# Kernel tuning notes

Hardware: AMD Instinct MI355X
Metric: run time of the kernel (lower is better)

## Reference

```python
import jax, jax.numpy as jnp
import numpy as np

B, N, C, H, PD, CLN = 8, 1024, 512, 8, 256, 64
HD = C // H
HID = 4 * C
LN_EPS = 1e-5
ATT_EPS = 1e-6


def layernorm(x, g, b):
    mu = x.mean(-1, keepdims=True)
    var = ((x - mu) ** 2).mean(-1, keepdims=True)
    return (x - mu) * jax.lax.rsqrt(var + LN_EPS) * g + b


def setup_inputs() -> dict:
    key = jax.random.key(0)
    ks = jax.random.split(key, 16)
    p = lambda k, shp, s=0.02: (jax.random.normal(k, shp, dtype=jnp.float32) * s)
    return {
        "x_token": jax.random.normal(ks[0], (B, N, C), dtype=jnp.float32),
        "x_path": jax.random.normal(ks[1], (B, N, PD), dtype=jnp.float32),
        "wq": p(ks[2], (C, C)),
        "wk": p(ks[3], (C, C)),
        "wv": p(ks[4], (C, C)),
        "w_proj": p(ks[5], (C, C)),
        "b_proj": jnp.zeros((C,), jnp.float32),
        "g1": jnp.ones((C,), jnp.float32),
        "b1": jnp.zeros((C,), jnp.float32),
        "g2": jnp.ones((C,), jnp.float32),
        "b2": jnp.zeros((C,), jnp.float32),
        "w1": p(ks[6], (HID, C)),
        "bb1": jnp.zeros((HID,), jnp.float32),
        "w2": p(ks[7], (C, HID)),
        "bb2": jnp.zeros((C,), jnp.float32),
        "idx_cluster": jax.random.randint(ks[8], (B, N), 0, CLN, dtype=jnp.int64 if jax.config.jax_enable_x64 else jnp.int32),
        "cluster_num": CLN,
    }


def reference(x_token, x_path, wq, wk, wv, w_proj, b_proj, g1, b1, g2, b2,
              w1, bb1, w2, bb2, idx_cluster, cluster_num):
    Bn, Nn, Cn = x_token.shape
    scale = (Cn // H) ** -0.5

    # norm1 + attention
    t = layernorm(x_token, g1, b1)
    q = (t @ wq.T).reshape(Bn, Nn, H, HD).transpose(0, 2, 1, 3)  # bhnd
    k = (t @ wk.T).reshape(Bn, Nn, H, HD).transpose(0, 2, 1, 3)
    v = (t @ wv.T).reshape(Bn, Nn, H, HD).transpose(0, 2, 1, 3)

    # scatter-to-(B,cluster,N,C) then sum over clusters == same-cluster mask on QK^T
    scores = jnp.einsum("bhid,bhjd->bhij", q, k) * scale  # (B,H,N,N)
    same = (idx_cluster[:, None, :, None] == idx_cluster[:, None, None, :])  # (B,1,N,N)
    scores = jnp.where(same, scores, jnp.float32(-1e9))

    # custom eps-stabilized exp-softmax (as in the torch code, no max-subtraction)
    e = jnp.exp(scores.astype(jnp.float32))
    attn = (e + ATT_EPS / Nn) / (e.sum(-1, keepdims=True) + ATT_EPS)

    out = jnp.einsum("bhij,bhjd->bhid", attn, v)
    out = out.transpose(0, 2, 1, 3).reshape(Bn, Nn, Cn)
    out = out @ w_proj.T + b_proj

    x = x_token + out  # drop_path is identity in eval

    # MLP block
    h = layernorm(x, g2, b2)
    m = jax.nn.gelu(h @ w1.T + bb1, approximate=False) @ w2.T + bb2
    return x + m
```

## Files before the change

kernel.cpp:

```cpp
#include <hip/hip_runtime.h>

typedef unsigned short u16;
typedef __attribute__((ext_vector_type(4))) float f32x4;
typedef __attribute__((ext_vector_type(8))) short s16x8;
typedef __attribute__((ext_vector_type(4))) unsigned short u16x4;
typedef __attribute__((ext_vector_type(8))) unsigned short u16x8;

__device__ __forceinline__ u16 f2bf(float f) {
    unsigned int u = __builtin_bit_cast(unsigned int, f);
    u += 0x7fffu + ((u >> 16) & 1u);
    return (u16)(u >> 16);
}
__device__ __forceinline__ float bf2f(u16 h) {
    unsigned int u = ((unsigned int)h) << 16;
    return __builtin_bit_cast(float, u);
}
__device__ __forceinline__ void gload16(const u16* g, u16* l) {
    __builtin_amdgcn_global_load_lds(
        (const __attribute__((address_space(1))) void*)g,
        (__attribute__((address_space(3))) void*)l, 16, 0, 0);
}
__device__ __forceinline__ float fgelu(float x) {
    float y = 0.7978845608f * (x + 0.044715f * x * x * x);
    float e = __builtin_amdgcn_exp2f(y * 2.8853900817f);
    float th = 1.0f - 2.0f / (1.0f + e);
    return 0.5f * x * (1.0f + th);
}

__global__ __launch_bounds__(256) void cvt_all(const float* __restrict__ wq,
                                               const float* __restrict__ wk,
                                               const float* __restrict__ wv,
                                               const float* __restrict__ wp,
                                               const float* __restrict__ w1,
                                               const float* __restrict__ w2,
                                               u16* __restrict__ dqkv,
                                               u16* __restrict__ dp,
                                               u16* __restrict__ dw1,
                                               u16* __restrict__ dw2,
                                               float* __restrict__ vsum) {
    int b = blockIdx.x;
    if (b >= 3072) {
        float4 z = {0.f, 0.f, 0.f, 0.f};
        ((float4*)vsum)[(b - 3072) * 256 + threadIdx.x] = z;
        return;
    }
    const float* src; u16* dst; int off;
    if      (b < 256)  { src = wq; dst = dqkv;          off = b; }
    else if (b < 512)  { src = wk; dst = dqkv + 262144; off = b - 256; }
    else if (b < 768)  { src = wv; dst = dqkv + 524288; off = b - 512; }
    else if (b < 1024) { src = wp; dst = dp;            off = b - 768; }
    else if (b < 2048) { src = w1; dst = dw1;           off = b - 1024; }
    else               { src = w2; dst = dw2;           off = b - 2048; }
    int i = off * 256 + threadIdx.x;
    float4 v = ((const float4*)src)[i];
    u16x4 o;
    o.x = f2bf(v.x); o.y = f2bf(v.y); o.z = f2bf(v.z); o.w = f2bf(v.w);
    ((u16x4*)dst)[i] = o;
}

__global__ __launch_bounds__(128) void ln_kernel(const float* __restrict__ in,
                                                 const float* __restrict__ g,
                                                 const float* __restrict__ bta,
                                                 u16* __restrict__ out) {
    int row = blockIdx.x;
    int t = threadIdx.x;
    float4 v = ((const float4*)(in + (size_t)row * 512))[t];
    float s  = v.x + v.y + v.z + v.w;
    float s2 = v.x * v.x + v.y * v.y + v.z * v.z + v.w * v.w;
#pragma unroll
    for (int m = 1; m < 64; m <<= 1) { s += __shfl_xor(s, m); s2 += __shfl_xor(s2, m); }
    __shared__ float sh[4];
    if ((t & 63) == 0) { sh[(t >> 6) * 2] = s; sh[(t >> 6) * 2 + 1] = s2; }
    __syncthreads();
    s = sh[0] + sh[2]; s2 = sh[1] + sh[3];
    float mu  = s * (1.0f / 512.0f);
    float var = s2 * (1.0f / 512.0f) - mu * mu;
    float rstd = rsqrtf(var + 1e-5f);
    float4 gv = ((const float4*)g)[t];
    float4 bv = ((const float4*)bta)[t];
    u16x4 o;
    o.x = f2bf((v.x - mu) * rstd * gv.x + bv.x);
    o.y = f2bf((v.y - mu) * rstd * gv.y + bv.y);
    o.z = f2bf((v.z - mu) * rstd * gv.z + bv.z);
    o.w = f2bf((v.w - mu) * rstd * gv.w + bv.w);
    ((u16x4*)(out + (size_t)row * 512))[t] = o;
}

__global__ __launch_bounds__(512) void vsum_part(const u16* __restrict__ qkv,
                                                 float* __restrict__ vsum) {
    int b = blockIdx.x >> 3, chunk = blockIdx.x & 7;
    int c = threadIdx.x;
    const u16* base = qkv + (size_t)b * 1024 * 1536 + 1024 + c;
    float s = 0.0f;
    for (int n = chunk * 128; n < chunk * 128 + 128; ++n) s += bf2f(base[(size_t)n * 1536]);
    atomicAdd(&vsum[b * 512 + c], s);
}

__global__ __launch_bounds__(1024) void cluster_sort(const int* __restrict__ idx,
                                                     int* __restrict__ perm,
                                                     int* __restrict__ cstart,
                                                     int* __restrict__ ccnt) {
    const int b = blockIdx.x, t = threadIdx.x;
    const int w = t >> 6, lane = t & 63;
    __shared__ int whist[16][64];
    __shared__ int cnt[64];
    __shared__ int off[64];
    ((int*)whist)[t] = 0;
    __syncthreads();
    const int myc = idx[b * 1024 + t];
    atomicAdd(&whist[w][myc], 1);
    int rank_w = 0;
    for (int c = 0; c < 64; ++c) {
        unsigned long long m = __ballot(myc == c);
        if (myc == c) rank_w = __popcll(m & ((1ull << lane) - 1ull));
    }
    __syncthreads();
    if (t < 64) {
        int s = 0;
        for (int ww = 0; ww < 16; ++ww) s += whist[ww][t];
        cnt[t] = s;
        ccnt[b * 64 + t] = s;
    }
    __syncthreads();
    if (t == 0) {
        int s = 0;
        for (int c = 0; c < 64; ++c) { off[c] = s; s += cnt[c]; }
    }
    __syncthreads();
    int cross = 0;
    for (int ww = 0; ww < w; ++ww) cross += whist[ww][myc];
    perm[b * 1024 + off[myc] + cross + rank_w] = t;
    if (t < 64) cstart[b * 64 + t] = off[t];
}

__global__ __launch_bounds__(64) void cattn_kernel(const u16* __restrict__ qkv,
                                                   const int* __restrict__ perm,
                                                   const int* __restrict__ cstart,
                                                   const int* __restrict__ ccnt,
                                                   const float* __restrict__ vsum,
                                                   u16* __restrict__ O) {
    const int bid = blockIdx.x;
    const int h = bid & 7, c = (bid >> 3) & 63, b = bid >> 9;
    const int m = ccnt[b * 64 + c];
    if (m == 0) return;
    const int start = b * 1024 + cstart[b * 64 + c];
    const int lane = threadIdx.x;
    const int fr = lane & 15, fkb = lane >> 4;
    __shared__ __align__(16) u16 Qs[16 * 72];
    __shared__ __align__(16) u16 Ks[32 * 72];
    __shared__ __align__(16) u16 Vt[64 * 36];
    __shared__ __align__(16) u16 Pl[16 * 40];

    const u16* qkv_b = qkv + (size_t)b * 1024 * 1536;
    const float epsN = 1e-6f / 1024.0f;

    for (int q0 = 0; q0 < m; q0 += 16) {
        __syncthreads();
        {
            int row = lane >> 3, seg = lane & 7;
#pragma unroll
            for (int p = 0; p < 2; ++p) {
                int r = row + p * 8;
                int gr = perm[start + min(q0 + r, m - 1)];
                *(int4*)(&Qs[r * 72 + seg * 8]) =
                    *(const int4*)(qkv_b + (size_t)gr * 1536 + h * 64 + seg * 8);
            }
        }
        __syncthreads();
        const s16x8 qf0 = *(const s16x8*)(&Qs[fr * 72 + fkb * 8]);
        const s16x8 qf1 = *(const s16x8*)(&Qs[fr * 72 + 32 + fkb * 8]);

        f32x4 oacc[4] = {};
        float rs[4] = {0.f, 0.f, 0.f, 0.f};

        for (int k0 = 0; k0 < m; k0 += 32) {
            __syncthreads();
            {
                int row = lane >> 3, seg = lane & 7;
#pragma unroll
                for (int p = 0; p < 4; ++p) {
                    int r = row + p * 8;
                    int gr = perm[start + min(k0 + r, m - 1)];
                    const u16* src = qkv_b + (size_t)gr * 1536 + h * 64 + seg * 8;
                    *(int4*)(&Ks[r * 72 + seg * 8]) = *(const int4*)(src + 512);
                    u16x8 vv = *(const u16x8*)(src + 1024);
#pragma unroll
                    for (int i = 0; i < 8; ++i) Vt[(seg * 8 + i) * 36 + r] = vv[i];
                }
            }
            __syncthreads();
#pragma unroll
            for (int ct = 0; ct < 2; ++ct) {
                f32x4 sacc = {};
                s16x8 kf0 = *(const s16x8*)(&Ks[(ct * 16 + fr) * 72 + fkb * 8]);
                s16x8 kf1 = *(const s16x8*)(&Ks[(ct * 16 + fr) * 72 + 32 + fkb * 8]);
                sacc = __builtin_amdgcn_mfma_f32_16x16x32_bf16(qf0, kf0, sacc, 0, 0, 0);
                sacc = __builtin_amdgcn_mfma_f32_16x16x32_bf16(qf1, kf1, sacc, 0, 0, 0);
                bool valid = (k0 + ct * 16 + fr) < m;
#pragma unroll
                for (int r = 0; r < 4; ++r) {
                    float e = valid ? __expf(sacc[r] * 0.125f) : 0.0f;
                    rs[r] += e;
                    Pl[(fkb * 4 + r) * 40 + ct * 16 + fr] = f2bf(e);
                }
            }
            __syncthreads();
            s16x8 pf = *(const s16x8*)(&Pl[fr * 40 + fkb * 8]);
#pragma unroll
            for (int dt = 0; dt < 4; ++dt) {
                s16x8 vf = *(const s16x8*)(&Vt[(dt * 16 + fr) * 36 + fkb * 8]);
                oacc[dt] = __builtin_amdgcn_mfma_f32_16x16x32_bf16(pf, vf, oacc[dt], 0, 0, 0);
            }
        }
#pragma unroll
        for (int r = 0; r < 4; ++r)
#pragma unroll
            for (int mm = 1; mm < 16; mm <<= 1) rs[r] += __shfl_xor(rs[r], mm);

#pragma unroll
        for (int r = 0; r < 4; ++r) {
            int ql = q0 + fkb * 4 + r;
            if (ql < m) {
                int orow = perm[start + ql];
#pragma unroll
                for (int dt = 0; dt < 4; ++dt) {
                    int dcol = dt * 16 + fr;
                    float vs = vsum[(b * 8 + h) * 64 + dcol];
                    float val = (oacc[dt][r] + epsN * vs) / (rs[r] + 1e-6f);
                    O[((size_t)(b * 1024 + orow)) * 512 + h * 64 + dcol] = f2bf(val);
                }
            }
        }
    }
}

template <int BM, bool OUT_BF16, bool BIAS, bool RESID, bool GELU>
__global__ __launch_bounds__(256) void gemm_sb(const u16* __restrict__ A,
                                               const u16* __restrict__ W,
                                               const float* __restrict__ bias,
                                               const float* __restrict__ resid,
                                               void* __restrict__ outp,
                                               int M, int N, int K) {
    constexpr int MI = BM / 32;
    __shared__ __align__(16) u16 As[BM * 64];
    __shared__ __align__(16) u16 Bs[128 * 64];
    const int bm = blockIdx.x, bn = blockIdx.y;
    const int t = threadIdx.x;
    const int lane = t & 63, w = t >> 6;
    const int wm = w >> 1, wn = w & 1;
    const int fr = lane & 15, fkb = lane >> 4;
    const int l8 = lane >> 3;
    const int c8s = (((lane & 7) ^ (l8 & 7)) * 8);
    f32x4 acc[MI][4] = {};
    const u16* Ab = A + (size_t)bm * BM * K;
    const u16* Wb = W + (size_t)bn * 128 * K;

    for (int k0 = 0; k0 < K; k0 += 64) {
        __syncthreads();
#pragma unroll
        for (int j = 0; j < MI; ++j) {
            int r = (w * MI + j) * 8 + l8;
            gload16(Ab + (size_t)r * K + k0 + c8s, &As[(w * MI + j) * 512]);
        }
#pragma unroll
        for (int j = 0; j < 4; ++j) {
            int r = (w * 4 + j) * 8 + l8;
            gload16(Wb + (size_t)r * K + k0 + c8s, &Bs[(w * 4 + j) * 512]);
        }
        __syncthreads();
#pragma unroll
        for (int kk = 0; kk < 64; kk += 32) {
            const int co = (((kk >> 3) + fkb) ^ (fr & 7)) << 3;
            s16x8 af[MI], bfv[4];
#pragma unroll
            for (int mi = 0; mi < MI; ++mi)
                af[mi] = *(const s16x8*)(&As[(wm * (BM / 2) + mi * 16 + fr) * 64 + co]);
#pragma unroll
            for (int ni = 0; ni < 4; ++ni)
                bfv[ni] = *(const s16x8*)(&Bs[(wn * 64 + ni * 16 + fr) * 64 + co]);
#pragma unroll
            for (int mi = 0; mi < MI; ++mi)
#pragma unroll
                for (int ni = 0; ni < 4; ++ni)
                    acc[mi][ni] = __builtin_amdgcn_mfma_f32_16x16x32_bf16(
                        bfv[ni], af[mi], acc[mi][ni], 0, 0, 0);
        }
    }

    const int rg = (lane >> 4) * 4;
#pragma unroll
    for (int mi = 0; mi < MI; ++mi) {
        const int grow = bm * BM + wm * (BM / 2) + mi * 16 + fr;
#pragma unroll
        for (int ni = 0; ni < 4; ++ni) {
            const int gcol = bn * 128 + wn * 64 + ni * 16 + rg;
            const size_t base = (size_t)grow * N + gcol;
            float4 v;
            v.x = acc[mi][ni][0]; v.y = acc[mi][ni][1];
            v.z = acc[mi][ni][2]; v.w = acc[mi][ni][3];
            if (BIAS) {
                float4 bv = *(const float4*)(bias + gcol);
                v.x += bv.x; v.y += bv.y; v.z += bv.z; v.w += bv.w;
            }
            if (GELU) {
                v.x = fgelu(v.x); v.y = fgelu(v.y); v.z = fgelu(v.z); v.w = fgelu(v.w);
            }
            if (RESID) {
                float4 rv = *(const float4*)(resid + base);
                v.x += rv.x; v.y += rv.y; v.z += rv.z; v.w += rv.w;
            }
            if (OUT_BF16) {
                u16x4 o;
                o.x = f2bf(v.x); o.y = f2bf(v.y); o.z = f2bf(v.z); o.w = f2bf(v.w);
                *(u16x4*)((u16*)outp + base) = o;
            } else {
                *(float4*)((float*)outp + base) = v;
            }
        }
    }
}

extern "C" void kernel_launch(void* const* d_in, const int* in_sizes, int n_in,
                              void* d_out, int out_size, void* d_ws, size_t ws_size,
                              hipStream_t stream) {
    const float* x_token = (const float*)d_in[0];
    const float* wq     = (const float*)d_in[2];
    const float* wk     = (const float*)d_in[3];
    const float* wv     = (const float*)d_in[4];
    const float* w_proj = (const float*)d_in[5];
    const float* b_proj = (const float*)d_in[6];
    const float* g1     = (const float*)d_in[7];
    const float* b1     = (const float*)d_in[8];
    const float* g2     = (const float*)d_in[9];
    const float* b2     = (const float*)d_in[10];
    const float* w1     = (const float*)d_in[11];
    const float* bb1    = (const float*)d_in[12];
    const float* w2     = (const float*)d_in[13];
    const float* bb2    = (const float*)d_in[14];
    const int*   idx    = (const int*)d_in[15];
    float* out_f = (float*)d_out;

    char* ws = (char*)d_ws;
    u16*   t_buf = (u16*)(ws);
    u16*   qkv   = (u16*)(ws + 8388608);
    u16*   Obuf  = (u16*)(ws + 8388608 + 25165824);
    u16*   m1    = qkv;
    float* xbuf  = (float*)(ws + 41943040);
    u16*   h_buf = t_buf;
    char*  wsw   = ws + 58720256;
    u16*   wqkv  = (u16*)(wsw);
    u16*   wprjb = (u16*)(wsw + 1572864);
    u16*   w1b   = (u16*)(wsw + 2097152);
    u16*   w2b   = (u16*)(wsw + 4194304);
    float* vsum  = (float*)(wsw + 6291456);
    int*   perm   = (int*)xbuf;
    int*   cstart = (int*)((char*)xbuf + 32768);
    int*   ccnt   = (int*)((char*)xbuf + 34816);
    (void)ws_size; (void)in_sizes; (void)n_in; (void)out_size;

    cvt_all<<<3076, 256, 0, stream>>>(wq, wk, wv, w_proj, w1, w2,
                                      wqkv, wprjb, w1b, w2b, vsum);
    cluster_sort<<<8, 1024, 0, stream>>>(idx, perm, cstart, ccnt);

    ln_kernel<<<8192, 128, 0, stream>>>(x_token, g1, b1, t_buf);
    gemm_sb<128, true, false, false, false><<<dim3(64, 12), 256, 0, stream>>>(
        t_buf, wqkv, nullptr, nullptr, qkv, 8192, 1536, 512);
    vsum_part<<<64, 512, 0, stream>>>(qkv, vsum);
    cattn_kernel<<<4096, 64, 0, stream>>>(qkv, perm, cstart, ccnt, vsum, Obuf);
    gemm_sb<64, false, true, true, false><<<dim3(128, 4), 256, 0, stream>>>(
        Obuf, wprjb, b_proj, x_token, xbuf, 8192, 512, 512);
    ln_kernel<<<8192, 128, 0, stream>>>(xbuf, g2, b2, h_buf);
    gemm_sb<128, true, true, false, true><<<dim3(64, 16), 256, 0, stream>>>(
        h_buf, w1b, bb1, nullptr, m1, 8192, 2048, 512);
    gemm_sb<64, false, true, true, false><<<dim3(128, 4), 256, 0, stream>>>(
        m1, w2b, bb2, xbuf, out_f, 8192, 512, 2048);
}
```

Baseline: 159.4 us.

## Split-K the final MLP GEMM with atomics and enlarge QKV/FC1 tiles

The final w2 GEMM now splits its K dimension in two over blockIdx.z and accumulates with float atomicAdd into an output that a new init kernel pre-fills with residual plus bias. The QKV and FC1 GEMMs move to 256-row tiles with half as many blocks. Split-K is meant to raise parallelism and bigger tiles to improve operand reuse. The trade-offs are more atomic traffic, an extra elementwise pass, fewer blocks for the enlarged GEMMs with more registers per thread, and sums whose order is no longer deterministic.

Result: slower. 285.8 us (+79.3%).

```diff
diff --git a/kernel.cpp b/kernel.cpp
--- a/kernel.cpp
+++ b/kernel.cpp
@@ -94,6 +94,16 @@
     float s = 0.0f;
     for (int n = chunk * 128; n < chunk * 128 + 128; ++n) s += bf2f(base[(size_t)n * 1536]);
     atomicAdd(&vsum[b * 512 + c], s);
+}
+
+__global__ __launch_bounds__(256) void init_out(const float* __restrict__ x,
+                                                const float* __restrict__ bb2,
+                                                float* __restrict__ out) {
+    int i = blockIdx.x * 256 + threadIdx.x;
+    float4 v = ((const float4*)x)[i];
+    float4 b = ((const float4*)bb2)[i & 127];
+    v.x += b.x; v.y += b.y; v.z += b.z; v.w += b.w;
+    ((float4*)out)[i] = v;
 }
 
 __global__ __launch_bounds__(1024) void cluster_sort(const int* __restrict__ idx,
@@ -234,13 +244,13 @@
     }
 }
 
-template <int BM, bool OUT_BF16, bool BIAS, bool RESID, bool GELU>
+template <int BM, bool OUT_BF16, bool BIAS, bool RESID, bool GELU, bool ATOMIC>
 __global__ __launch_bounds__(256) void gemm_sb(const u16* __restrict__ A,
                                                const u16* __restrict__ W,
                                                const float* __restrict__ bias,
                                                const float* __restrict__ resid,
                                                void* __restrict__ outp,
-                                               int M, int N, int K) {
+                                               int M, int N, int K, int KS) {
     constexpr int MI = BM / 32;
     __shared__ __align__(16) u16 As[BM * 64];
     __shared__ __align__(16) u16 Bs[128 * 64];
@@ -248,14 +258,16 @@
     const int t = threadIdx.x;
     const int lane = t & 63, w = t >> 6;
     const int wm = w >> 1, wn = w & 1;
-    const int fr = lane & 15, fkb = lane >> 4;
+    const int fr = lane & 15;
     const int l8 = lane >> 3;
     const int c8s = (((lane & 7) ^ (l8 & 7)) * 8);
+    const int fkb = lane >> 4;
     f32x4 acc[MI][4] = {};
-    const u16* Ab = A + (size_t)bm * BM * K;
-    const u16* Wb = W + (size_t)bn * 128 * K;
-
-    for (int k0 = 0; k0 < K; k0 += 64) {
+    const size_t kbase = (size_t)blockIdx.z * KS;
+    const u16* Ab = A + (size_t)bm * BM * K + kbase;
+    const u16* Wb = W + (size_t)bn * 128 * K + kbase;
+
+    for (int k0 = 0; k0 < KS; k0 += 64) {
         __syncthreads();
 #pragma unroll
         for (int j = 0; j < MI; ++j) {
@@ -309,7 +321,13 @@
                 float4 rv = *(const float4*)(resid + base);
                 v.x += rv.x; v.y += rv.y; v.z += rv.z; v.w += rv.w;
             }
-            if (OUT_BF16) {
+            if (ATOMIC) {
+                float* o = (float*)outp + base;
+                atomicAdd(o + 0, v.x);
+                atomicAdd(o + 1, v.y);
+                atomicAdd(o + 2, v.z);
+                atomicAdd(o + 3, v.w);
+            } else if (OUT_BF16) {
                 u16x4 o;
                 o.x = f2bf(v.x); o.y = f2bf(v.y); o.z = f2bf(v.z); o.w = f2bf(v.w);
                 *(u16x4*)((u16*)outp + base) = o;
@@ -363,15 +381,16 @@
     cluster_sort<<<8, 1024, 0, stream>>>(idx, perm, cstart, ccnt);
 
     ln_kernel<<<8192, 128, 0, stream>>>(x_token, g1, b1, t_buf);
-    gemm_sb<128, true, false, false, false><<<dim3(64, 12), 256, 0, stream>>>(
-        t_buf, wqkv, nullptr, nullptr, qkv, 8192, 1536, 512);
+    gemm_sb<256, true, false, false, false, false><<<dim3(32, 12), 256, 0, stream>>>(
+        t_buf, wqkv, nullptr, nullptr, qkv, 8192, 1536, 512, 512);
     vsum_part<<<64, 512, 0, stream>>>(qkv, vsum);
     cattn_kernel<<<4096, 64, 0, stream>>>(qkv, perm, cstart, ccnt, vsum, Obuf);
-    gemm_sb<64, false, true, true, false><<<dim3(128, 4), 256, 0, stream>>>(
-        Obuf, wprjb, b_proj, x_token, xbuf, 8192, 512, 512);
+    gemm_sb<64, false, true, true, false, false><<<dim3(128, 4), 256, 0, stream>>>(
+        Obuf, wprjb, b_proj, x_token, xbuf, 8192, 512, 512, 512);
     ln_kernel<<<8192, 128, 0, stream>>>(xbuf, g2, b2, h_buf);
-    gemm_sb<128, true, true, false, true><<<dim3(64, 16), 256, 0, stream>>>(
-        h_buf, w1b, bb1, nullptr, m1, 8192, 2048, 512);
-    gemm_sb<64, false, true, true, false><<<dim3(128, 4), 256, 0, stream>>>(
-        m1, w2b, bb2, xbuf, out_f, 8192, 512, 2048);
-}
+    gemm_sb<256, true, true, false, true, false><<<dim3(32, 16), 256, 0, stream>>>(
+        h_buf, w1b, bb1, nullptr, m1, 8192, 2048, 512, 512);
+    init_out<<<4096, 256, 0, stream>>>(xbuf, bb2, out_f);
+    gemm_sb<128, false, false, false, false, true><<<dim3(64, 4, 2), 256, 0, stream>>>(
+        m1, w2b, nullptr, nullptr, out_f, 8192, 512, 2048, 1024);
+}
```
